# Optimization experiments

Hardware: AMD Instinct MI355X
Metric: run time of the kernel (lower is better)

Reference implementation:

```python
import jax, jax.numpy as jnp
import numpy as np

N_T, N_C, N_M = 300000, 100000, 20000
D_IN, D, D_OUT = 390, 128, 64
H_PRE, H_POST = 256, 64


def _nrm(k, shape, scale=0.02):
    return jax.random.normal(k, shape, dtype=jnp.float32) * scale


def setup_inputs() -> dict:
    key = jax.random.key(0)
    ks = jax.random.split(key, 24)
    inp = {
        'input_features': jax.random.normal(ks[0], (N_T, D_IN), jnp.float32),
        'card_of_target': jax.random.randint(ks[1], (N_T,), 0, N_C, jnp.int32),
        'merchant_of_target': jax.random.randint(ks[2], (N_T,), 0, N_M, jnp.int32),
        # HeteroEmbedding tables for src types feeding 'target'
        'card_emb': _nrm(ks[3], (N_C, D)),
        'merch_emb': _nrm(ks[4], (N_M, D)),
        # target_preprocessing FFBlock (390 -> 256 -> 128, n_layers=2)
        'pre_Wi': _nrm(ks[5], (D_IN, H_PRE)), 'pre_bi': jnp.zeros((H_PRE,), jnp.float32),
        'pre_Wh': _nrm(ks[6], (H_PRE, H_PRE)), 'pre_bh': jnp.zeros((H_PRE,), jnp.float32),
        'pre_Wo': _nrm(ks[7], (H_PRE, D)), 'pre_bo': jnp.zeros((D,), jnp.float32),
        # conv1 / conv2: one GraphConv per etype; order:
        # 0=card->target, 1=merchant->target, 2=target->card, 3=target->merchant
        'conv1_W': _nrm(ks[8], (4, D, D)), 'conv1_b': jnp.zeros((4, D), jnp.float32),
        'conv2_W': _nrm(ks[9], (4, D, D)), 'conv2_b': jnp.zeros((4, D), jnp.float32),
        # conv3: dst=='target' -> D_OUT; dst!='target' -> 1
        'conv3_Wt': _nrm(ks[10], (2, D, D_OUT)), 'conv3_bt': jnp.zeros((2, D_OUT), jnp.float32),
        'conv3_Wo': _nrm(ks[11], (2, D, 1)), 'conv3_bo': jnp.zeros((2, 1), jnp.float32),
        # target_postprocessing FFBlock (64 -> 64 -> 1, n_layers=2)
        'post_Wi': _nrm(ks[12], (D_OUT, H_POST)), 'post_bi': jnp.zeros((H_POST,), jnp.float32),
        'post_Wh': _nrm(ks[13], (H_POST, H_POST)), 'post_bh': jnp.zeros((H_POST,), jnp.float32),
        'post_Wo': _nrm(ks[14], (H_POST, 1)), 'post_bo': jnp.zeros((1,), jnp.float32),
    }
    return inp


def _ff(x, Wi, bi, Wh, bh, Wo, bo, n_layers=2):
    h = jax.nn.relu(x @ Wi + bi)
    for _ in range(1, n_layers):
        h = jax.nn.relu(h @ Wh + bh)
    return h @ Wo + bo


def _deg(ids, n):
    # degree per node over edge endpoint list, clamped to >= 1 (DGL GraphConv)
    return jnp.maximum(jnp.zeros((n,), jnp.float32).at[ids].add(1.0), 1.0)


def _gconv(x_src, src, dst, n_dst, W, b, d_src, d_dst):
    # DGL GraphConv, norm='both': scale src by out_deg^-1/2, matmul,
    # sum messages onto dst, scale by in_deg^-1/2, add bias.
    h = (x_src * jax.lax.rsqrt(d_src)[:, None]) @ W          # [n_src, out]
    agg = jax.ops.segment_sum(h[src], dst, num_segments=n_dst)
    return agg * jax.lax.rsqrt(d_dst)[:, None] + b


def reference(input_features, card_of_target, merchant_of_target,
              card_emb, merch_emb,
              pre_Wi, pre_bi, pre_Wh, pre_bh, pre_Wo, pre_bo,
              conv1_W, conv1_b, conv2_W, conv2_b,
              conv3_Wt, conv3_bt, conv3_Wo, conv3_bo,
              post_Wi, post_bi, post_Wh, post_bh, post_Wo, post_bo):
    n_t, n_c, n_m = input_features.shape[0], card_emb.shape[0], merch_emb.shape[0]
    t_ids = jnp.arange(n_t, dtype=jnp.int32)
    d_c = _deg(card_of_target, n_c)      # card degree (in/out symmetric here)
    d_m = _deg(merchant_of_target, n_m)  # merchant degree
    d_t = _deg(t_ids, n_t)               # target degree (=1 per etype)

    tf = _ff(input_features, pre_Wi, pre_bi, pre_Wh, pre_bh, pre_Wo, pre_bo)

    # conv1 (HeteroGraphConv, aggregate='sum') + relu
    h1_t = (_gconv(card_emb, card_of_target, t_ids, n_t, conv1_W[0], conv1_b[0], d_c, d_t)
            + _gconv(merch_emb, merchant_of_target, t_ids, n_t, conv1_W[1], conv1_b[1], d_m, d_t))
    h1_c = _gconv(tf, t_ids, card_of_target, n_c, conv1_W[2], conv1_b[2], d_t, d_c)
    h1_m = _gconv(tf, t_ids, merchant_of_target, n_m, conv1_W[3], conv1_b[3], d_t, d_m)
    h1_t, h1_c, h1_m = jax.nn.relu(h1_t), jax.nn.relu(h1_c), jax.nn.relu(h1_m)

    # conv2 applied (conv_layers - 2) = 1 time
    h2_t, h2_c, h2_m = h1_t, h1_c, h1_m
    for _ in range(2, 3):
        n_t2 = (_gconv(h2_c, card_of_target, t_ids, n_t, conv2_W[0], conv2_b[0], d_c, d_t)
                + _gconv(h2_m, merchant_of_target, t_ids, n_t, conv2_W[1], conv2_b[1], d_m, d_t))
        n_c2 = _gconv(h2_t, t_ids, card_of_target, n_c, conv2_W[2], conv2_b[2], d_t, d_c)
        n_m2 = _gconv(h2_t, t_ids, merchant_of_target, n_m, conv2_W[3], conv2_b[3], d_t, d_m)
        h2_t, h2_c, h2_m = jax.nn.relu(n_t2), jax.nn.relu(n_c2), jax.nn.relu(n_m2)

    # conv3: D_OUT into target, 1 into non-target dsts; no relu
    h3_t = (_gconv(h2_c, card_of_target, t_ids, n_t, conv3_Wt[0], conv3_bt[0], d_c, d_t)
            + _gconv(h2_m, merchant_of_target, t_ids, n_t, conv3_Wt[1], conv3_bt[1], d_m, d_t))
    h3_c = _gconv(h2_t, t_ids, card_of_target, n_c, conv3_Wo[0], conv3_bo[0], d_t, d_c)
    h3_m = _gconv(h2_t, t_ids, merchant_of_target, n_m, conv3_Wo[1], conv3_bo[1], d_t, d_m)

    h3_t = _ff(h3_t, post_Wi, post_bi, post_Wh, post_bh, post_Wo, post_bo)
    return h3_t, h3_c, h3_m
```

## Files before the change

### kernel.cpp

```cpp
#include <hip/hip_runtime.h>


#define NT 300000
#define NC 100000
#define NM 20000
#define DIN 390
#define DD 128
#define DOUT 64
#define HPRE 256
#define HPOST 64

typedef _Float16 half8 __attribute__((ext_vector_type(8)));
typedef _Float16 half4v __attribute__((ext_vector_type(4)));
typedef float f32x16 __attribute__((ext_vector_type(16)));
typedef float f32x4 __attribute__((ext_vector_type(4)));

#define LO_SCALE 512.0f
#define LO_INV   (1.0f / 512.0f)

__device__ __forceinline__ void split2(float x, _Float16& h, _Float16& l) {
    _Float16 hh = (_Float16)x;
    h = hh;
    l = (_Float16)((x - (float)hh) * LO_SCALE);
}

__device__ __forceinline__ void gload16(const _Float16* g, _Float16* l) {
    __builtin_amdgcn_global_load_lds(
        (const __attribute__((address_space(1))) void*)g,
        (__attribute__((address_space(3))) void*)l, 16, 0, 0);
}

template<int TN>
__global__ __launch_bounds__(512, 4) void gemm_ps(
    const _Float16* __restrict__ Agh, const _Float16* __restrict__ Agl,
    const _Float16* __restrict__ Bgh, const _Float16* __restrict__ Bgl,
    const float* __restrict__ bias, const float* __restrict__ rowscale,
    _Float16* __restrict__ Ch, _Float16* __restrict__ Cl,
    float* __restrict__ C32,
    int M, int Kpad, int N, int relu)
{
    constexpr int BM = 128;
    constexpr int BN = 64 * TN;
    constexpr int BHALF = BN * 32;
    constexpr int BUFB  = 2 * BHALF;
    constexpr int OFF_B = 24576;
    __shared__ __align__(16) _Float16 smem[OFF_B + 2 * BUFB];

    const int tid  = (int)threadIdx.x;
    const int lane = tid & 63;
    const int wave = tid >> 6;
    const int wm0  = (wave & 3) * 32;
    const int wn0  = (wave >> 2) * 32 * TN;

    const int nbn  = N / BN;
    const int bm   = ((int)blockIdx.x / nbn) * BM;
    const int bn   = ((int)blockIdx.x % nbn) * BN;

    const int srow = lane >> 2;
    const int xc8  = (((lane & 3) ^ ((srow >> 1) & 3)) << 3);
    const size_t a_off = (size_t)(bm + wave * 16 + srow) * Kpad + xc8;
    size_t b_off;
    if constexpr (TN == 2) {
        b_off = (size_t)(bn + wave * 16 + srow) * Kpad + xc8;
    } else {
        b_off = (size_t)(bn + (wave & 3) * 16 + srow) * Kpad + xc8;
    }

    auto stageA = [&](int ab, int k0) {
        _Float16* base = &smem[ab * 8192];
        gload16(Agh + a_off + k0, base + wave * 512);
        gload16(Agl + a_off + k0, base + 4096 + wave * 512);
    };
    auto stageB = [&](int bb, int k0) {
        _Float16* base = &smem[OFF_B + bb * BUFB];
        if constexpr (TN == 2) {
            gload16(Bgh + b_off + k0, base + wave * 512);
            gload16(Bgl + b_off + k0, base + BHALF + wave * 512);
        } else {
            gload16((wave < 4 ? Bgh : Bgl) + b_off + k0,
                    base + (wave < 4 ? 0 : BHALF) + (wave & 3) * 512);
        }
    };

    f32x16 zz;
    #pragma unroll
    for (int i = 0; i < 16; ++i) zz[i] = 0.f;
    f32x16 acc_hh[TN], acc_x[TN];
    #pragma unroll
    for (int t2 = 0; t2 < TN; ++t2) { acc_hh[t2] = zz; acc_x[t2] = zz; }

    const int mlr = lane & 31;
    const int hi5 = lane >> 5;
    const int xr  = (mlr >> 1) & 3;

    const int NS = Kpad >> 5;

    stageB(0, 0);
    stageA(0, 0);
    if (NS > 1) stageA(1, 32);

    int ca = 0, cn = 2;

    for (int t = 0; t < NS; ++t) {
        if (t + 1 < NS) stageB((t + 1) & 1, (t + 1) << 5);
        if (t + 2 < NS) stageA(cn, (t + 2) << 5);

        if (t + 2 < NS) {
            asm volatile("s_waitcnt vmcnt(%0)" :: "n"(TN == 2 ? 6 : 5) : "memory");
        } else if (t + 1 < NS) {
            asm volatile("s_waitcnt vmcnt(%0)" :: "n"(TN == 2 ? 4 : 3) : "memory");
        } else {
            asm volatile("s_waitcnt vmcnt(0)" ::: "memory");
        }
        __builtin_amdgcn_s_barrier();
        __builtin_amdgcn_sched_barrier(0);

        const _Float16* sa = &smem[ca * 8192];
        const _Float16* sb = &smem[OFF_B + (t & 1) * BUFB];
        #pragma unroll
        for (int ks = 0; ks < 2; ++ks) {
            const int xo = (((ks * 2 + hi5) ^ xr) << 3);
            const half8 fah = *(const half8*)&sa[(wm0 + mlr) * 32 + xo];
            const half8 fal = *(const half8*)&sa[4096 + (wm0 + mlr) * 32 + xo];
            half8 fbh[TN], fbl[TN];
            #pragma unroll
            for (int t2 = 0; t2 < TN; ++t2) {
                const int nn = wn0 + t2 * 32 + mlr;
                fbh[t2] = *(const half8*)&sb[nn * 32 + xo];
                fbl[t2] = *(const half8*)&sb[BHALF + nn * 32 + xo];
            }
            #pragma unroll
            for (int t2 = 0; t2 < TN; ++t2) {
                acc_hh[t2] = __builtin_amdgcn_mfma_f32_32x32x16_f16(
                    fah, fbh[t2], acc_hh[t2], 0, 0, 0);
                acc_x[t2] = __builtin_amdgcn_mfma_f32_32x32x16_f16(
                    fah, fbl[t2], acc_x[t2], 0, 0, 0);
                acc_x[t2] = __builtin_amdgcn_mfma_f32_32x32x16_f16(
                    fal, fbh[t2], acc_x[t2], 0, 0, 0);
            }
        }
        __builtin_amdgcn_sched_barrier(0);
        __builtin_amdgcn_s_barrier();

        ca = (ca == 2) ? 0 : ca + 1;
        cn = (cn == 2) ? 0 : cn + 1;
    }

    const int r0 = 4 * hi5;
    #pragma unroll
    for (int t2 = 0; t2 < TN; ++t2) {
        const int gcol = bn + wn0 + t2 * 32 + mlr;
        const float bc = (bias != nullptr) ? bias[gcol] : 0.f;
        #pragma unroll
        for (int r = 0; r < 16; ++r) {
            const int grow = bm + wm0 + (r & 3) + r0 + 8 * (r >> 2);
            if (grow < M) {
                float v = acc_hh[t2][r] + acc_x[t2][r] * LO_INV;
                if (rowscale != nullptr) v *= rowscale[grow];
                v += bc;
                if (relu) v = fmaxf(v, 0.f);
                if (C32 != nullptr) {
                    C32[(size_t)grow * N + gcol] = v;
                } else {
                    _Float16 hh, ll;
                    split2(v, hh, ll);
                    Ch[(size_t)grow * N + gcol] = hh;
                    Cl[(size_t)grow * N + gcol] = ll;
                }
            }
        }
    }
}

template<int TM, int TN, int WGM, int WGN>
__global__ __launch_bounds__(256, 3) void gemm_mfma(
    const float* __restrict__ A, const _Float16* __restrict__ Wh,
    const _Float16* __restrict__ Wl, const float* __restrict__ bias,
    const float* __restrict__ rowscale,
    float* __restrict__ C32, _Float16* __restrict__ Ch, _Float16* __restrict__ Cl,
    int M, int K, int N, int Kpad, int relu)
{
    constexpr int BM = 32 * TM * WGM;
    constexpr int BN = 32 * TN * WGN;
    constexpr int RS = 40;
    __shared__ __align__(16) _Float16 Ah[BM * RS];
    __shared__ __align__(16) _Float16 Al[BM * RS];
    __shared__ __align__(16) _Float16 Bh[BN * RS];
    __shared__ __align__(16) _Float16 Bl[BN * RS];

    const int tid  = (int)threadIdx.x;
    const int lane = tid & 63;
    const int wave = tid >> 6;
    const int wm0 = (wave % WGM) * 32 * TM;
    const int wn0 = (wave / WGM) * 32 * TN;

    const int nbn = N / BN;
    const int tile = (int)blockIdx.x;
    const int bm = (tile / nbn) * BM;
    const int bn = (tile % nbn) * BN;

    f32x16 zz;
    #pragma unroll
    for (int i = 0; i < 16; ++i) zz[i] = 0.f;
    f32x16 acc_hh[TM][TN], acc_x[TM][TN];
    #pragma unroll
    for (int tm = 0; tm < TM; ++tm)
        #pragma unroll
        for (int tn = 0; tn < TN; ++tn) { acc_hh[tm][tn] = zz; acc_x[tm][tn] = zz; }

    constexpr int TPR  = 256 / BM;
    constexpr int KPT  = 32 / TPR;
    constexpr int FQ   = KPT / 4;
    const int sar = tid / TPR;
    const int sak = (tid % TPR) * KPT;
    const int agrow = bm + sar;
    const float* Aptr = A + (size_t)agrow * K;

    constexpr int TPRB = 256 / BN;
    constexpr int KPTB = 32 / TPRB;
    constexpr int NB   = KPTB / 8;
    const int sbr = tid / TPRB;
    const int sbk = (tid % TPRB) * KPTB;
    const _Float16* Bhp = Wh + (size_t)(bn + sbr) * Kpad + sbk;
    const _Float16* Blp = Wl + (size_t)(bn + sbr) * Kpad + sbk;

    const int ml  = lane & 31;
    const int klo = (lane >> 5) * 8;

    f32x4 areg0[FQ], areg1[FQ];
    half8 bh0[NB], bl0[NB], bh1[NB], bl1[NB];

    auto loadA = [&](f32x4 (&ar)[FQ], int k0) {
        #pragma unroll
        for (int q = 0; q < FQ; ++q) {
            const int kb = k0 + sak + q * 4;
            f32x4 f = {0.f, 0.f, 0.f, 0.f};
            if (agrow < M) {
                if (kb + 3 < K) {
                    f = *(const f32x4*)(Aptr + kb);
                } else {
                    if (kb + 0 < K) f[0] = Aptr[kb + 0];
                    if (kb + 1 < K) f[1] = Aptr[kb + 1];
                    if (kb + 2 < K) f[2] = Aptr[kb + 2];
                    if (kb + 3 < K) f[3] = Aptr[kb + 3];
                }
            }
            ar[q] = f;
        }
    };
    auto loadB = [&](half8 (&bh)[NB], half8 (&bl)[NB], int k0) {
        #pragma unroll
        for (int j = 0; j < NB; ++j) {
            bh[j] = *(const half8*)(Bhp + k0 + j * 8);
            bl[j] = *(const half8*)(Blp + k0 + j * 8);
        }
    };

    loadA(areg0, 0);
    loadB(bh0, bl0, 0);
    if (32 < K) { loadA(areg1, 32); loadB(bh1, bl1, 32); }

    auto step = [&](f32x4 (&ar)[FQ], half8 (&bh)[NB], half8 (&bl)[NB], int k0) {
        #pragma unroll
        for (int c = 0; c < FQ / 2; ++c) {
            half8 h, l;
            #pragma unroll
            for (int q = 0; q < 2; ++q) {
                #pragma unroll
                for (int j = 0; j < 4; ++j) {
                    _Float16 th, tl;
                    split2(ar[2 * c + q][j], th, tl);
                    h[q * 4 + j] = th;
                    l[q * 4 + j] = tl;
                }
            }
            *(half8*)&Ah[sar * RS + sak + c * 8] = h;
            *(half8*)&Al[sar * RS + sak + c * 8] = l;
        }
        #pragma unroll
        for (int j = 0; j < NB; ++j) {
            *(half8*)&Bh[sbr * RS + sbk + j * 8] = bh[j];
            *(half8*)&Bl[sbr * RS + sbk + j * 8] = bl[j];
        }
        __syncthreads();

        if (k0 + 64 < K) { loadA(ar, k0 + 64); loadB(bh, bl, k0 + 64); }

        #pragma unroll
        for (int ks = 0; ks < 2; ++ks) {
            const int kk = ks * 16 + klo;
            half8 fah[TM], fal[TM], fbh[TN], fbl[TN];
            #pragma unroll
            for (int t = 0; t < TM; ++t) {
                const int m = wm0 + t * 32 + ml;
                fah[t] = *(const half8*)&Ah[m * RS + kk];
                fal[t] = *(const half8*)&Al[m * RS + kk];
            }
            #pragma unroll
            for (int t = 0; t < TN; ++t) {
                const int n = wn0 + t * 32 + ml;
                fbh[t] = *(const half8*)&Bh[n * RS + kk];
                fbl[t] = *(const half8*)&Bl[n * RS + kk];
            }
            #pragma unroll
            for (int tm = 0; tm < TM; ++tm)
                #pragma unroll
                for (int tn = 0; tn < TN; ++tn) {
                    acc_hh[tm][tn] = __builtin_amdgcn_mfma_f32_32x32x16_f16(
                        fah[tm], fbh[tn], acc_hh[tm][tn], 0, 0, 0);
                    acc_x[tm][tn] = __builtin_amdgcn_mfma_f32_32x32x16_f16(
                        fah[tm], fbl[tn], acc_x[tm][tn], 0, 0, 0);
                    acc_x[tm][tn] = __builtin_amdgcn_mfma_f32_32x32x16_f16(
                        fal[tm], fbh[tn], acc_x[tm][tn], 0, 0, 0);
                }
        }
        __syncthreads();
    };

    for (int k0 = 0; k0 < K; k0 += 64) {
        step(areg0, bh0, bl0, k0);
        if (k0 + 32 < K) step(areg1, bh1, bl1, k0 + 32);
    }

    const int r0 = 4 * (lane >> 5);
    #pragma unroll
    for (int tm = 0; tm < TM; ++tm) {
        #pragma unroll
        for (int tn = 0; tn < TN; ++tn) {
            const int gcol = bn + wn0 + tn * 32 + ml;
            const float bc = (bias != nullptr) ? bias[gcol] : 0.f;
            #pragma unroll
            for (int r = 0; r < 16; ++r) {
                const int grow = bm + wm0 + tm * 32 + (r & 3) + r0 + 8 * (r >> 2);
                if (grow < M) {
                    float v = acc_hh[tm][tn][r] + acc_x[tm][tn][r] * LO_INV;
                    if (rowscale != nullptr) v *= rowscale[grow];
                    v += bc;
                    if (relu) v = fmaxf(v, 0.f);
                    if (C32 != nullptr) {
                        C32[(size_t)grow * N + gcol] = v;
                    } else {
                        _Float16 hh, ll;
                        split2(v, hh, ll);
                        Ch[(size_t)grow * N + gcol] = hh;
                        Cl[(size_t)grow * N + gcol] = ll;
                    }
                }
            }
        }
    }
}

__global__ __launch_bounds__(512, 2) void post_ff(
    const float* __restrict__ hc, const float* __restrict__ hm,
    const int* __restrict__ card, const int* __restrict__ merch,
    const float* __restrict__ bt0, const float* __restrict__ bt1,
    const _Float16* __restrict__ wih, const _Float16* __restrict__ wil,
    const float* __restrict__ bi,
    const _Float16* __restrict__ whh, const _Float16* __restrict__ whl,
    const float* __restrict__ bh,
    const float* __restrict__ wo, const float* __restrict__ bo,
    float* __restrict__ out, int n)
{
    constexpr int SR = 72;
    constexpr int OFF_AH = 0;
    constexpr int OFF_AL = 9216;
    constexpr int OFF_HH = 18432;
    constexpr int OFF_HL = 27648;
    constexpr int OFF_W1H = 36864;
    constexpr int OFF_W1L = 41472;
    constexpr int OFF_W2H = 46080;
    constexpr int OFF_W2L = 50688;
    __shared__ __align__(16) _Float16 S[55296];
    float* sh2 = (float*)&S[OFF_AH];

    const int tid  = (int)threadIdx.x;
    const int lane = tid & 63;
    const int wave = tid >> 6;
    const int bm   = (int)blockIdx.x * 128;

    {
        const int wn = (tid & 255) >> 2;
        const int c0 = (tid & 3) * 16;
        const _Float16* gh = (tid < 256) ? wih : whh;
        const _Float16* gl = (tid < 256) ? wil : whl;
        const int oh = (tid < 256) ? OFF_W1H : OFF_W2H;
        const int ol = (tid < 256) ? OFF_W1L : OFF_W2L;
        *(half8*)&S[oh + wn * SR + c0]     = *(const half8*)(gh + wn * 64 + c0);
        *(half8*)&S[oh + wn * SR + c0 + 8] = *(const half8*)(gh + wn * 64 + c0 + 8);
        *(half8*)&S[ol + wn * SR + c0]     = *(const half8*)(gl + wn * 64 + c0);
        *(half8*)&S[ol + wn * SR + c0 + 8] = *(const half8*)(gl + wn * 64 + c0 + 8);
    }
    {
        const int r  = tid >> 2;
        const int c0 = (tid & 3) << 4;
        const int t  = bm + r;
        const bool ok = (t < n);
        const int ci = ok ? card[t] : 0;
        const int mi = ok ? merch[t] : 0;
        #pragma unroll
        for (int q = 0; q < 4; ++q) {
            const int c = c0 + q * 4;
            float4 a = make_float4(0.f, 0.f, 0.f, 0.f);
            if (ok) {
                float4 va = *(const float4*)(hc + (size_t)ci * 64 + c);
                float4 vb = *(const float4*)(hm + (size_t)mi * 64 + c);
                float4 b0 = *(const float4*)(bt0 + c);
                float4 b1 = *(const float4*)(bt1 + c);
                a.x = va.x + vb.x + b0.x + b1.x;
                a.y = va.y + vb.y + b0.y + b1.y;
                a.z = va.z + vb.z + b0.z + b1.z;
                a.w = va.w + vb.w + b0.w + b1.w;
            }
            half4v h, l;
            _Float16 th, tl;
            split2(a.x, th, tl); h[0] = th; l[0] = tl;
            split2(a.y, th, tl); h[1] = th; l[1] = tl;
            split2(a.z, th, tl); h[2] = th; l[2] = tl;
            split2(a.w, th, tl); h[3] = th; l[3] = tl;
            *(half4v*)&S[OFF_AH + r * SR + c] = h;
            *(half4v*)&S[OFF_AL + r * SR + c] = l;
        }
    }
    __syncthreads();

    const int mlr = lane & 31;
    const int hi5 = lane >> 5;
    const int wm = (wave & 3) * 32;
    const int wn = (wave >> 2) * 32;
    const int r0 = 4 * hi5;

    f32x16 zz;
    #pragma unroll
    for (int i = 0; i < 16; ++i) zz[i] = 0.f;

    {
        f32x16 acc = zz, accx = zz;
        #pragma unroll
        for (int ks = 0; ks < 4; ++ks) {
            const int kk = ks * 16 + hi5 * 8;
            const half8 fah = *(const half8*)&S[OFF_AH + (wm + mlr) * SR + kk];
            const half8 fal = *(const half8*)&S[OFF_AL + (wm + mlr) * SR + kk];
            const half8 fbh = *(const half8*)&S[OFF_W1H + (wn + mlr) * SR + kk];
            const half8 fbl = *(const half8*)&S[OFF_W1L + (wn + mlr) * SR + kk];
            acc  = __builtin_amdgcn_mfma_f32_32x32x16_f16(fah, fbh, acc, 0, 0, 0);
            accx = __builtin_amdgcn_mfma_f32_32x32x16_f16(fah, fbl, accx, 0, 0, 0);
            accx = __builtin_amdgcn_mfma_f32_32x32x16_f16(fal, fbh, accx, 0, 0, 0);
        }
        const float bc = bi[wn + mlr];
        __syncthreads();
        #pragma unroll
        for (int r = 0; r < 16; ++r) {
            const int row = wm + (r & 3) + r0 + 8 * (r >> 2);
            float v = acc[r] + accx[r] * LO_INV + bc;
            v = fmaxf(v, 0.f);
            _Float16 hh, ll;
            split2(v, hh, ll);
            S[OFF_HH + row * SR + wn + mlr] = hh;
            S[OFF_HL + row * SR + wn + mlr] = ll;
        }
    }
    __syncthreads();

    {
        f32x16 acc = zz, accx = zz;
        #pragma unroll
        for (int ks = 0; ks < 4; ++ks) {
            const int kk = ks * 16 + hi5 * 8;
            const half8 fah = *(const half8*)&S[OFF_HH + (wm + mlr) * SR + kk];
            const half8 fal = *(const half8*)&S[OFF_HL + (wm + mlr) * SR + kk];
            const half8 fbh = *(const half8*)&S[OFF_W2H + (wn + mlr) * SR + kk];
            const half8 fbl = *(const half8*)&S[OFF_W2L + (wn + mlr) * SR + kk];
            acc  = __builtin_amdgcn_mfma_f32_32x32x16_f16(fah, fbh, acc, 0, 0, 0);
            accx = __builtin_amdgcn_mfma_f32_32x32x16_f16(fah, fbl, accx, 0, 0, 0);
            accx = __builtin_amdgcn_mfma_f32_32x32x16_f16(fal, fbh, accx, 0, 0, 0);
        }
        const float bc = bh[wn + mlr];
        __syncthreads();
        #pragma unroll
        for (int r = 0; r < 16; ++r) {
            const int row = wm + (r & 3) + r0 + 8 * (r >> 2);
            float v = acc[r] + accx[r] * LO_INV + bc;
            sh2[row * 68 + wn + mlr] = fmaxf(v, 0.f);
        }
    }
    __syncthreads();

    if (tid < 128) {
        const int t = bm + tid;
        if (t < n) {
            float s = bo[0];
            #pragma unroll 8
            for (int c = 0; c < 64; ++c) s += sh2[tid * 68 + c] * wo[c];
            out[t] = s;
        }
    }
}

__global__ void split_w(const float* __restrict__ W, _Float16* __restrict__ hiT,
                        _Float16* __restrict__ loT, int K, int N, int Kpad, int nmat)
{
    int idx = blockIdx.x * blockDim.x + threadIdx.x;
    int total = nmat * N * Kpad;
    if (idx >= total) return;
    int e = idx / (N * Kpad);
    int rem = idx - e * (N * Kpad);
    int n = rem / Kpad;
    int k = rem - n * Kpad;
    float v = (k < K) ? W[((size_t)e * K + k) * N + n] : 0.f;
    _Float16 h = (_Float16)v;
    hiT[idx] = h;
    loT[idx] = (_Float16)((v - (float)h) * LO_SCALE);
}

__global__ void split_a(const float* __restrict__ X, _Float16* __restrict__ xh,
                        _Float16* __restrict__ xl, int M, int Mpad, int K)
{
    int idx = blockIdx.x * blockDim.x + threadIdx.x;
    int per = K >> 3;
    int total = Mpad * per;
    if (idx >= total) return;
    int row = idx / per;
    int k = (idx - row * per) << 3;
    half8 h, l;
    if (row < M) {
        #pragma unroll
        for (int j = 0; j < 8; ++j) {
            _Float16 th, tl;
            split2(X[(size_t)row * K + k + j], th, tl);
            h[j] = th; l[j] = tl;
        }
    } else {
        #pragma unroll
        for (int j = 0; j < 8; ++j) { h[j] = (_Float16)0.f; l[j] = (_Float16)0.f; }
    }
    *(half8*)&xh[(size_t)row * K + k] = h;
    *(half8*)&xl[(size_t)row * K + k] = l;
}

__global__ void count_kernel(const int* __restrict__ card, const int* __restrict__ merch,
                             int* cnt_c, int* cnt_m, int n)
{
    int t = blockIdx.x * blockDim.x + threadIdx.x;
    if (t >= n) return;
    atomicAdd(&cnt_c[card[t]], 1);
    atomicAdd(&cnt_m[merch[t]], 1);
}

__global__ void rsqrt_kernel(const int* __restrict__ cnt, float* __restrict__ rs, int n)
{
    int i = blockIdx.x * blockDim.x + threadIdx.x;
    if (i >= n) return;
    int c = cnt[i];
    if (c < 1) c = 1;
    rs[i] = 1.0f / sqrtf((float)c);
}

__global__ __launch_bounds__(1024) void scan_excl(const int* __restrict__ cnt,
                                                  int* __restrict__ off, int n)
{
    __shared__ int wsum[16];
    const int tid = (int)threadIdx.x;
    const int lane = tid & 63, wid = tid >> 6;
    int carry = 0;
    for (int base = 0; base < n; base += 1024) {
        int i = base + tid;
        int v = (i < n) ? cnt[i] : 0;
        int x = v;
        #pragma unroll
        for (int d = 1; d < 64; d <<= 1) {
            int y = __shfl_up(x, d);
            if (lane >= d) x += y;
        }
        if (lane == 63) wsum[wid] = x;
        __syncthreads();
        int wpre = 0, tot = 0;
        #pragma unroll
        for (int w = 0; w < 16; ++w) {
            int s = wsum[w];
            if (w < wid) wpre += s;
            tot += s;
        }
        if (i < n) off[i] = carry + wpre + (x - v);
        carry += tot;
        __syncthreads();
    }
    if (tid == 0) off[n] = carry;
}

__global__ void fill_sorted(const int* __restrict__ ids, const int* __restrict__ off,
                            int* cur, int* __restrict__ srt, int n)
{
    int t = blockIdx.x * blockDim.x + threadIdx.x;
    if (t >= n) return;
    int c = ids[t];
    int p = atomicAdd(&cur[c], 1);
    srt[off[c] + p] = t;
}

__global__ void gather2_kernel(const float* __restrict__ hc, const float* __restrict__ hm,
                               const int* __restrict__ card, const int* __restrict__ merch,
                               const float* __restrict__ b0, const float* __restrict__ b1,
                               float* __restrict__ out32, _Float16* __restrict__ oh,
                               _Float16* __restrict__ ol, int n, int dim, int relu)
{
    int idx = blockIdx.x * blockDim.x + threadIdx.x;
    int per = dim >> 2;
    int t = idx / per;
    if (t >= n) return;
    int d4 = (idx % per) << 2;
    int c = card[t], m = merch[t];
    float4 a = *(const float4*)(hc + (size_t)c * dim + d4);
    float4 b = *(const float4*)(hm + (size_t)m * dim + d4);
    float4 v0 = *(const float4*)(b0 + d4);
    float4 v1 = *(const float4*)(b1 + d4);
    float4 r;
    r.x = a.x + b.x + v0.x + v1.x;
    r.y = a.y + b.y + v0.y + v1.y;
    r.z = a.z + b.z + v0.z + v1.z;
    r.w = a.w + b.w + v0.w + v1.w;
    if (relu) {
        r.x = fmaxf(r.x, 0.f); r.y = fmaxf(r.y, 0.f);
        r.z = fmaxf(r.z, 0.f); r.w = fmaxf(r.w, 0.f);
    }
    if (out32 != nullptr) {
        *(float4*)(out32 + (size_t)t * dim + d4) = r;
    } else {
        half4v h, l;
        _Float16 th, tl;
        split2(r.x, th, tl); h[0] = th; l[0] = tl;
        split2(r.y, th, tl); h[1] = th; l[1] = tl;
        split2(r.z, th, tl); h[2] = th; l[2] = tl;
        split2(r.w, th, tl); h[3] = th; l[3] = tl;
        *(half4v*)&oh[(size_t)t * dim + d4] = h;
        *(half4v*)&ol[(size_t)t * dim + d4] = l;
    }
}

__global__ __launch_bounds__(256) void agg_csr_kernel(
    const float* __restrict__ proj, int ldp, int doff,
    const int* __restrict__ off, const int* __restrict__ srt,
    const float* __restrict__ rs, const float* __restrict__ bias,
    _Float16* __restrict__ oh, _Float16* __restrict__ ol, int n, int relu)
{
    int node = blockIdx.x * 2 + ((int)threadIdx.x >> 7);
    int d = (int)threadIdx.x & 127;
    if (node >= n) return;
    int s = off[node], e = off[node + 1];
    float acc = 0.f;
    for (int i = s; i < e; ++i) {
        int t = srt[i];
        acc += proj[(size_t)t * ldp + doff + d];
    }
    float v = acc * rs[node] + bias[d];
    if (relu) v = fmaxf(v, 0.f);
    _Float16 hh, ll;
    split2(v, hh, ll);
    oh[(size_t)node * 128 + d] = hh;
    ol[(size_t)node * 128 + d] = ll;
}

__global__ __launch_bounds__(256) void dot2_kernel(
    const float* __restrict__ h, const float* __restrict__ w0,
    const float* __restrict__ w1, float* __restrict__ s2, int n)
{
    int row = blockIdx.x * 4 + ((int)threadIdx.x >> 6);
    int l = (int)threadIdx.x & 63;
    if (row >= n) return;
    const float* x = h + (size_t)row * 128;
    float x0 = x[l], x1 = x[l + 64];
    float p0 = x0 * w0[l] + x1 * w0[l + 64];
    float p1 = x0 * w1[l] + x1 * w1[l + 64];
    #pragma unroll
    for (int o = 32; o > 0; o >>= 1) {
        p0 += __shfl_down(p0, o);
        p1 += __shfl_down(p1, o);
    }
    if (l == 0) { s2[(size_t)row * 2] = p0; s2[(size_t)row * 2 + 1] = p1; }
}

__global__ void agg_scalar_kernel(const float* __restrict__ s2, int which,
                                  const int* __restrict__ off, const int* __restrict__ srt,
                                  const float* __restrict__ rs, const float* __restrict__ bias,
                                  float* __restrict__ out, int n)
{
    int node = blockIdx.x * blockDim.x + threadIdx.x;
    if (node >= n) return;
    float acc = 0.f;
    int e = off[node + 1];
    for (int i = off[node]; i < e; ++i) acc += s2[(size_t)srt[i] * 2 + which];
    out[node] = acc * rs[node] + bias[0];
}

static inline void gemm_ps_launch(const _Float16* Ah, const _Float16* Al,
    const _Float16* Bh, const _Float16* Bl, const float* bias, const float* rs,
    _Float16* Ch, _Float16* Cl, float* C32,
    int M, int Kpad, int N, int relu, hipStream_t s)
{
    const int nbm = (M + 127) / 128;
    if (N % 128 == 0) {
        gemm_ps<2><<<dim3(nbm * (N / 128)), 512, 0, s>>>(
            Ah, Al, Bh, Bl, bias, rs, Ch, Cl, C32, M, Kpad, N, relu);
    } else {
        gemm_ps<1><<<dim3(nbm), 512, 0, s>>>(
            Ah, Al, Bh, Bl, bias, rs, Ch, Cl, C32, M, Kpad, N, relu);
    }
}

#define PAD128(x) ((((x) + 127) / 128) * 128)

extern "C" void kernel_launch(void* const* d_in, const int* in_sizes, int n_in,
                              void* d_out, int out_size, void* d_ws, size_t ws_size,
                              hipStream_t stream)
{
    const float* x_in      = (const float*)d_in[0];
    const int*   card      = (const int*)d_in[1];
    const int*   merch     = (const int*)d_in[2];
    const float* card_emb  = (const float*)d_in[3];
    const float* merch_emb = (const float*)d_in[4];
    const float* pre_Wi = (const float*)d_in[5];
    const float* pre_bi = (const float*)d_in[6];
    const float* pre_Wh = (const float*)d_in[7];
    const float* pre_bh = (const float*)d_in[8];
    const float* pre_Wo = (const float*)d_in[9];
    const float* pre_bo = (const float*)d_in[10];
    const float* conv1_W = (const float*)d_in[11];
    const float* conv1_b = (const float*)d_in[12];
    const float* conv2_W = (const float*)d_in[13];
    const float* conv2_b = (const float*)d_in[14];
    const float* conv3_Wt = (const float*)d_in[15];
    const float* conv3_bt = (const float*)d_in[16];
    const float* conv3_Wo = (const float*)d_in[17];
    const float* conv3_bo = (const float*)d_in[18];
    const float* post_Wi = (const float*)d_in[19];
    const float* post_bi = (const float*)d_in[20];
    const float* post_Wh = (const float*)d_in[21];
    const float* post_bh = (const float*)d_in[22];
    const float* post_Wo = (const float*)d_in[23];
    const float* post_bo = (const float*)d_in[24];

    float* out = (float*)d_out;

    const int MTP = PAD128(NT);
    const int MCP = PAD128(NC);
    const int MMP = PAD128(NM);

    char* ws = (char*)d_ws;
    size_t off = 0;
    auto alloc = [&](size_t bytes) -> char* {
        char* p = ws + off;
        off += (bytes + 255) & ~(size_t)255;
        return p;
    };
    int* cnt_c = (int*)alloc((size_t)NC * 4);
    int* cnt_m = (int*)alloc((size_t)NM * 4);
    int* cur_c = (int*)alloc((size_t)NC * 4);
    int* cur_m = (int*)alloc((size_t)NM * 4);
    size_t zero_bytes = (size_t)((char*)(cur_m + NM) - (char*)cnt_c);
    int* off_c = (int*)alloc((size_t)(NC + 1) * 4);
    int* off_m = (int*)alloc((size_t)(NM + 1) * 4);
    int* srt_c = (int*)alloc((size_t)NT * 4);
    int* srt_m = (int*)alloc((size_t)NT * 4);
    float* rs_c = (float*)alloc((size_t)NC * 4);
    float* rs_m = (float*)alloc((size_t)NM * 4);

    const int KP_WI = 416;
    _Float16* wi_h  = (_Float16*)alloc((size_t)HPRE * KP_WI * 2);
    _Float16* wi_l  = (_Float16*)alloc((size_t)HPRE * KP_WI * 2);
    _Float16* wh_h  = (_Float16*)alloc((size_t)HPRE * HPRE * 2);
    _Float16* wh_l  = (_Float16*)alloc((size_t)HPRE * HPRE * 2);
    _Float16* wo_h  = (_Float16*)alloc((size_t)DD * HPRE * 2);
    _Float16* wo_l  = (_Float16*)alloc((size_t)DD * HPRE * 2);
    _Float16* c1_h  = (_Float16*)alloc((size_t)4 * DD * DD * 2);
    _Float16* c1_l  = (_Float16*)alloc((size_t)4 * DD * DD * 2);
    _Float16* c2_h  = (_Float16*)alloc((size_t)4 * DD * DD * 2);
    _Float16* c2_l  = (_Float16*)alloc((size_t)4 * DD * DD * 2);
    _Float16* c3_h  = (_Float16*)alloc((size_t)2 * DOUT * DD * 2);
    _Float16* c3_l  = (_Float16*)alloc((size_t)2 * DOUT * DD * 2);
    _Float16* pi_h  = (_Float16*)alloc((size_t)HPOST * DOUT * 2);
    _Float16* pi_l  = (_Float16*)alloc((size_t)HPOST * DOUT * 2);
    _Float16* ph_h  = (_Float16*)alloc((size_t)HPOST * HPOST * 2);
    _Float16* ph_l  = (_Float16*)alloc((size_t)HPOST * HPOST * 2);

    _Float16* ce_h   = (_Float16*)alloc((size_t)MCP * DD * 2);
    _Float16* ce_l   = (_Float16*)alloc((size_t)MCP * DD * 2);
    _Float16* me_h   = (_Float16*)alloc((size_t)MMP * DD * 2);
    _Float16* me_l   = (_Float16*)alloc((size_t)MMP * DD * 2);
    _Float16* bufA_h = (_Float16*)alloc((size_t)MTP * HPRE * 2);
    _Float16* bufA_l = (_Float16*)alloc((size_t)MTP * HPRE * 2);
    _Float16* bufB_h = (_Float16*)alloc((size_t)MTP * HPRE * 2);
    _Float16* bufB_l = (_Float16*)alloc((size_t)MTP * HPRE * 2);
    _Float16* tf_h   = (_Float16*)alloc((size_t)MTP * DD * 2);
    _Float16* tf_l   = (_Float16*)alloc((size_t)MTP * DD * 2);
    _Float16* h1t_h  = (_Float16*)alloc((size_t)MTP * DD * 2);
    _Float16* h1t_l  = (_Float16*)alloc((size_t)MTP * DD * 2);
    _Float16* h1c_h  = (_Float16*)alloc((size_t)MCP * DD * 2);
    _Float16* h1c_l  = (_Float16*)alloc((size_t)MCP * DD * 2);
    _Float16* h1m_h  = (_Float16*)alloc((size_t)MMP * DD * 2);
    _Float16* h1m_l  = (_Float16*)alloc((size_t)MMP * DD * 2);
    _Float16* h2c_h  = (_Float16*)alloc((size_t)MCP * DD * 2);
    _Float16* h2c_l  = (_Float16*)alloc((size_t)MCP * DD * 2);
    _Float16* h2m_h  = (_Float16*)alloc((size_t)MMP * DD * 2);
    _Float16* h2m_l  = (_Float16*)alloc((size_t)MMP * DD * 2);

    float* proj = (float*)alloc((size_t)MTP * 256 * 4);
    float* h2_t = (float*)alloc((size_t)MTP * DD * 4);
    float* hc_p = (float*)alloc((size_t)MCP * DD * 4);
    float* hm_p = (float*)alloc((size_t)MMP * DD * 4);
    float* s2   = (float*)alloc((size_t)NT * 2 * 4);
    (void)ws_size; (void)in_sizes; (void)n_in; (void)out_size;

    hipMemsetAsync(cnt_c, 0, zero_bytes, stream);
    count_kernel<<<(NT + 255) / 256, 256, 0, stream>>>(card, merch, cnt_c, cnt_m, NT);
    rsqrt_kernel<<<(NC + 255) / 256, 256, 0, stream>>>(cnt_c, rs_c, NC);
    rsqrt_kernel<<<(NM + 255) / 256, 256, 0, stream>>>(cnt_m, rs_m, NM);
    scan_excl<<<1, 1024, 0, stream>>>(cnt_c, off_c, NC);
    scan_excl<<<1, 1024, 0, stream>>>(cnt_m, off_m, NM);
    fill_sorted<<<(NT + 255) / 256, 256, 0, stream>>>(card, off_c, cur_c, srt_c, NT);
    fill_sorted<<<(NT + 255) / 256, 256, 0, stream>>>(merch, off_m, cur_m, srt_m, NT);

    auto splitw = [&](const float* W, _Float16* h, _Float16* l, int K, int N, int Kpad, int nmat) {
        int total = nmat * N * Kpad;
        split_w<<<(total + 255) / 256, 256, 0, stream>>>(W, h, l, K, N, Kpad, nmat);
    };
    splitw(pre_Wi,   wi_h, wi_l, DIN,  HPRE,  KP_WI, 1);
    splitw(pre_Wh,   wh_h, wh_l, HPRE, HPRE,  HPRE,  1);
    splitw(pre_Wo,   wo_h, wo_l, HPRE, DD,    HPRE,  1);
    splitw(conv1_W,  c1_h, c1_l, DD,   DD,    DD,    4);
    splitw(conv2_W,  c2_h, c2_l, DD,   DD,    DD,    4);
    splitw(conv3_Wt, c3_h, c3_l, DD,   DOUT,  DD,    2);
    splitw(post_Wi,  pi_h, pi_l, DOUT, HPOST, DOUT,  1);
    splitw(post_Wh,  ph_h, ph_l, HPOST,HPOST, HPOST, 1);

    split_a<<<((MCP * (DD / 8)) + 255) / 256, 256, 0, stream>>>(card_emb, ce_h, ce_l, NC, MCP, DD);
    split_a<<<((MMP * (DD / 8)) + 255) / 256, 256, 0, stream>>>(merch_emb, me_h, me_l, NM, MMP, DD);

    const int WP  = DD * DD;
    const int WP3 = DOUT * DD;

    {
        const int nbm = (NT + 63) / 64;
        gemm_mfma<1, 2, 2, 2><<<dim3(nbm * 2), 256, 0, stream>>>(
            x_in, wi_h, wi_l, pre_bi, nullptr, nullptr, bufA_h, bufA_l,
            NT, DIN, HPRE, KP_WI, 1);
    }
    gemm_ps_launch(bufA_h, bufA_l, wh_h, wh_l, pre_bh, nullptr,
                   bufB_h, bufB_l, nullptr, NT, HPRE, HPRE, 1, stream);
    gemm_ps_launch(bufB_h, bufB_l, wo_h, wo_l, pre_bo, nullptr,
                   tf_h, tf_l, nullptr, NT, HPRE, DD, 0, stream);

    gemm_ps_launch(ce_h, ce_l, c1_h + 0 * WP, c1_l + 0 * WP, nullptr, rs_c,
                   nullptr, nullptr, hc_p, NC, DD, DD, 0, stream);
    gemm_ps_launch(me_h, me_l, c1_h + 1 * WP, c1_l + 1 * WP, nullptr, rs_m,
                   nullptr, nullptr, hm_p, NM, DD, DD, 0, stream);
    gather2_kernel<<<(NT * (DD / 4) + 255) / 256, 256, 0, stream>>>(
        hc_p, hm_p, card, merch, conv1_b, conv1_b + DD,
        nullptr, h1t_h, h1t_l, NT, DD, 1);
    gemm_ps_launch(tf_h, tf_l, c1_h + 2 * WP, c1_l + 2 * WP, nullptr, nullptr,
                   nullptr, nullptr, proj, NT, DD, 256, 0, stream);
    agg_csr_kernel<<<(NC + 1) / 2, 256, 0, stream>>>(proj, 256, 0, off_c, srt_c, rs_c,
                                                     conv1_b + 2 * DD, h1c_h, h1c_l, NC, 1);
    agg_csr_kernel<<<(NM + 1) / 2, 256, 0, stream>>>(proj, 256, 128, off_m, srt_m, rs_m,
                                                     conv1_b + 3 * DD, h1m_h, h1m_l, NM, 1);

    gemm_ps_launch(h1c_h, h1c_l, c2_h + 0 * WP, c2_l + 0 * WP, nullptr, rs_c,
                   nullptr, nullptr, hc_p, NC, DD, DD, 0, stream);
    gemm_ps_launch(h1m_h, h1m_l, c2_h + 1 * WP, c2_l + 1 * WP, nullptr, rs_m,
                   nullptr, nullptr, hm_p, NM, DD, DD, 0, stream);
    gather2_kernel<<<(NT * (DD / 4) + 255) / 256, 256, 0, stream>>>(
        hc_p, hm_p, card, merch, conv2_b, conv2_b + DD,
        h2_t, nullptr, nullptr, NT, DD, 1);
    gemm_ps_launch(h1t_h, h1t_l, c2_h + 2 * WP, c2_l + 2 * WP, nullptr, nullptr,
                   nullptr, nullptr, proj, NT, DD, 256, 0, stream);
    agg_csr_kernel<<<(NC + 1) / 2, 256, 0, stream>>>(proj, 256, 0, off_c, srt_c, rs_c,
                                                     conv2_b + 2 * DD, h2c_h, h2c_l, NC, 1);
    agg_csr_kernel<<<(NM + 1) / 2, 256, 0, stream>>>(proj, 256, 128, off_m, srt_m, rs_m,
                                                     conv2_b + 3 * DD, h2m_h, h2m_l, NM, 1);

    gemm_ps_launch(h2c_h, h2c_l, c3_h + 0 * WP3, c3_l + 0 * WP3, nullptr, rs_c,
                   nullptr, nullptr, hc_p, NC, DD, DOUT, 0, stream);
    gemm_ps_launch(h2m_h, h2m_l, c3_h + 1 * WP3, c3_l + 1 * WP3, nullptr, rs_m,
                   nullptr, nullptr, hm_p, NM, DD, DOUT, 0, stream);
    dot2_kernel<<<(NT + 3) / 4, 256, 0, stream>>>(h2_t, conv3_Wo, conv3_Wo + DD, s2, NT);
    agg_scalar_kernel<<<(NC + 255) / 256, 256, 0, stream>>>(s2, 0, off_c, srt_c, rs_c,
                                                            conv3_bo + 0, out + NT, NC);
    agg_scalar_kernel<<<(NM + 255) / 256, 256, 0, stream>>>(s2, 1, off_m, srt_m, rs_m,
                                                            conv3_bo + 1, out + NT + NC, NM);

    post_ff<<<dim3((NT + 127) / 128), 512, 0, stream>>>(
        hc_p, hm_p, card, merch, conv3_bt, conv3_bt + DOUT,
        pi_h, pi_l, post_bi, ph_h, ph_l, post_bh, post_Wo, post_bo, out, NT);
}
```

Baseline: 2.796 ms.

## Aggregate target features before projecting for card/merchant convs, simplify GEMM pipelines

For the target->card and target->merchant graph convolutions, the raw target features are now summed over each destination node's edges first and then multiplied by the weight, instead of projecting all 300k target rows and aggregating the projections. This swaps a 300k-row GEMM with N=256 for two GEMMs over 100k and 20k rows, with bias, row scale and relu applied in the GEMM epilogue. The gathers now read 128-wide fp32 rows and the target features are stored as fp32 rather than split fp16 pairs. Separately, both GEMM kernels drop from triple/double-buffered register and LDS pipelining to a plain double buffer, which may expose more load latency.

```diff
diff --git a/kernel.cpp b/kernel.cpp
--- a/kernel.cpp
+++ b/kernel.cpp
@@ -41,10 +41,12 @@
 {
     constexpr int BM = 128;
     constexpr int BN = 64 * TN;
-    constexpr int BHALF = BN * 32;
-    constexpr int BUFB  = 2 * BHALF;
-    constexpr int OFF_B = 24576;
-    __shared__ __align__(16) _Float16 smem[OFF_B + 2 * BUFB];
+    constexpr int OFF_AL = 4096;
+    constexpr int OFF_BH = 8192;
+    constexpr int OFF_BL = 8192 + BN * 32;
+    constexpr int BUFH   = 8192 + 2 * BN * 32;
+    constexpr int NLD    = (TN == 2) ? 4 : 3;
+    __shared__ __align__(16) _Float16 smem[2 * BUFH];
 
     const int tid  = (int)threadIdx.x;
     const int lane = tid & 63;
@@ -66,19 +68,16 @@
         b_off = (size_t)(bn + (wave & 3) * 16 + srow) * Kpad + xc8;
     }
 
-    auto stageA = [&](int ab, int k0) {
-        _Float16* base = &smem[ab * 8192];
-        gload16(Agh + a_off + k0, base + wave * 512);
-        gload16(Agl + a_off + k0, base + 4096 + wave * 512);
-    };
-    auto stageB = [&](int bb, int k0) {
-        _Float16* base = &smem[OFF_B + bb * BUFB];
+    auto stage = [&](int b, int k0) {
+        _Float16* sb = &smem[b * BUFH];
+        gload16(Agh + a_off + k0, sb + wave * 512);
+        gload16(Agl + a_off + k0, sb + OFF_AL + wave * 512);
         if constexpr (TN == 2) {
-            gload16(Bgh + b_off + k0, base + wave * 512);
-            gload16(Bgl + b_off + k0, base + BHALF + wave * 512);
+            gload16(Bgh + b_off + k0, sb + OFF_BH + wave * 512);
+            gload16(Bgl + b_off + k0, sb + OFF_BL + wave * 512);
         } else {
             gload16((wave < 4 ? Bgh : Bgl) + b_off + k0,
-                    base + (wave < 4 ? 0 : BHALF) + (wave & 3) * 512);
+                    sb + (wave < 4 ? OFF_BH : OFF_BL) + (wave & 3) * 512);
         }
     };
 
@@ -94,40 +93,30 @@
     const int xr  = (mlr >> 1) & 3;
 
     const int NS = Kpad >> 5;
-
-    stageB(0, 0);
-    stageA(0, 0);
-    if (NS > 1) stageA(1, 32);
-
-    int ca = 0, cn = 2;
+    stage(0, 0);
 
     for (int t = 0; t < NS; ++t) {
-        if (t + 1 < NS) stageB((t + 1) & 1, (t + 1) << 5);
-        if (t + 2 < NS) stageA(cn, (t + 2) << 5);
-
-        if (t + 2 < NS) {
-            asm volatile("s_waitcnt vmcnt(%0)" :: "n"(TN == 2 ? 6 : 5) : "memory");
-        } else if (t + 1 < NS) {
-            asm volatile("s_waitcnt vmcnt(%0)" :: "n"(TN == 2 ? 4 : 3) : "memory");
+        if (t + 1 < NS) {
+            stage((t + 1) & 1, (t + 1) << 5);
+            asm volatile("s_waitcnt vmcnt(%0)" :: "n"(NLD) : "memory");
         } else {
             asm volatile("s_waitcnt vmcnt(0)" ::: "memory");
         }
         __builtin_amdgcn_s_barrier();
         __builtin_amdgcn_sched_barrier(0);
 
-        const _Float16* sa = &smem[ca * 8192];
-        const _Float16* sb = &smem[OFF_B + (t & 1) * BUFB];
+        const _Float16* sb = &smem[(t & 1) * BUFH];
         #pragma unroll
         for (int ks = 0; ks < 2; ++ks) {
             const int xo = (((ks * 2 + hi5) ^ xr) << 3);
-            const half8 fah = *(const half8*)&sa[(wm0 + mlr) * 32 + xo];
-            const half8 fal = *(const half8*)&sa[4096 + (wm0 + mlr) * 32 + xo];
+            const half8 fah = *(const half8*)&sb[(wm0 + mlr) * 32 + xo];
+            const half8 fal = *(const half8*)&sb[OFF_AL + (wm0 + mlr) * 32 + xo];
             half8 fbh[TN], fbl[TN];
             #pragma unroll
             for (int t2 = 0; t2 < TN; ++t2) {
                 const int nn = wn0 + t2 * 32 + mlr;
-                fbh[t2] = *(const half8*)&sb[nn * 32 + xo];
-                fbl[t2] = *(const half8*)&sb[BHALF + nn * 32 + xo];
+                fbh[t2] = *(const half8*)&sb[OFF_BH + nn * 32 + xo];
+                fbl[t2] = *(const half8*)&sb[OFF_BL + nn * 32 + xo];
             }
             #pragma unroll
             for (int t2 = 0; t2 < TN; ++t2) {
@@ -141,9 +130,6 @@
         }
         __builtin_amdgcn_sched_barrier(0);
         __builtin_amdgcn_s_barrier();
-
-        ca = (ca == 2) ? 0 : ca + 1;
-        cn = (cn == 2) ? 0 : cn + 1;
     }
 
     const int r0 = 4 * hi5;
@@ -227,10 +213,10 @@
     const int ml  = lane & 31;
     const int klo = (lane >> 5) * 8;
 
-    f32x4 areg0[FQ], areg1[FQ];
-    half8 bh0[NB], bl0[NB], bh1[NB], bl1[NB];
-
-    auto loadA = [&](f32x4 (&ar)[FQ], int k0) {
+    f32x4 areg[FQ];
+    half8 bhreg[NB], blreg[NB];
+
+    auto loadA = [&](int k0) {
         #pragma unroll
         for (int q = 0; q < FQ; ++q) {
             const int kb = k0 + sak + q * 4;
@@ -245,22 +231,21 @@
                     if (kb + 3 < K) f[3] = Aptr[kb + 3];
                 }
             }
-            ar[q] = f;
+            areg[q] = f;
         }
     };
-    auto loadB = [&](half8 (&bh)[NB], half8 (&bl)[NB], int k0) {
+    auto loadB = [&](int k0) {
         #pragma unroll
         for (int j = 0; j < NB; ++j) {
-            bh[j] = *(const half8*)(Bhp + k0 + j * 8);
-            bl[j] = *(const half8*)(Blp + k0 + j * 8);
+            bhreg[j] = *(const half8*)(Bhp + k0 + j * 8);
+            blreg[j] = *(const half8*)(Blp + k0 + j * 8);
         }
     };
 
-    loadA(areg0, 0);
-    loadB(bh0, bl0, 0);
-    if (32 < K) { loadA(areg1, 32); loadB(bh1, bl1, 32); }
-
-    auto step = [&](f32x4 (&ar)[FQ], half8 (&bh)[NB], half8 (&bl)[NB], int k0) {
+    loadA(0);
+    loadB(0);
+
+    for (int k0 = 0; k0 < K; k0 += 32) {
         #pragma unroll
         for (int c = 0; c < FQ / 2; ++c) {
             half8 h, l;
@@ -269,7 +254,7 @@
                 #pragma unroll
                 for (int j = 0; j < 4; ++j) {
                     _Float16 th, tl;
-                    split2(ar[2 * c + q][j], th, tl);
+                    split2(areg[2 * c + q][j], th, tl);
                     h[q * 4 + j] = th;
                     l[q * 4 + j] = tl;
                 }
@@ -279,12 +264,12 @@
         }
         #pragma unroll
         for (int j = 0; j < NB; ++j) {
-            *(half8*)&Bh[sbr * RS + sbk + j * 8] = bh[j];
-            *(half8*)&Bl[sbr * RS + sbk + j * 8] = bl[j];
+            *(half8*)&Bh[sbr * RS + sbk + j * 8] = bhreg[j];
+            *(half8*)&Bl[sbr * RS + sbk + j * 8] = blreg[j];
         }
         __syncthreads();
 
-        if (k0 + 64 < K) { loadA(ar, k0 + 64); loadB(bh, bl, k0 + 64); }
+        if (k0 + 32 < K) { loadA(k0 + 32); loadB(k0 + 32); }
 
         #pragma unroll
         for (int ks = 0; ks < 2; ++ks) {
@@ -315,11 +300,6 @@
                 }
         }
         __syncthreads();
-    };
-
-    for (int k0 = 0; k0 < K; k0 += 64) {
-        step(areg0, bh0, bl0, k0);
-        if (k0 + 32 < K) step(areg1, bh1, bl1, k0 + 32);
     }
 
     const int r0 = 4 * (lane >> 5);
@@ -601,8 +581,7 @@
 __global__ void gather2_kernel(const float* __restrict__ hc, const float* __restrict__ hm,
                                const int* __restrict__ card, const int* __restrict__ merch,
                                const float* __restrict__ b0, const float* __restrict__ b1,
-                               float* __restrict__ out32, _Float16* __restrict__ oh,
-                               _Float16* __restrict__ ol, int n, int dim, int relu)
+                               float* __restrict__ out, int n, int dim, int relu)
 {
     int idx = blockIdx.x * blockDim.x + threadIdx.x;
     int per = dim >> 2;
@@ -623,39 +602,23 @@
         r.x = fmaxf(r.x, 0.f); r.y = fmaxf(r.y, 0.f);
         r.z = fmaxf(r.z, 0.f); r.w = fmaxf(r.w, 0.f);
     }
-    if (out32 != nullptr) {
-        *(float4*)(out32 + (size_t)t * dim + d4) = r;
-    } else {
-        half4v h, l;
-        _Float16 th, tl;
-        split2(r.x, th, tl); h[0] = th; l[0] = tl;
-        split2(r.y, th, tl); h[1] = th; l[1] = tl;
-        split2(r.z, th, tl); h[2] = th; l[2] = tl;
-        split2(r.w, th, tl); h[3] = th; l[3] = tl;
-        *(half4v*)&oh[(size_t)t * dim + d4] = h;
-        *(half4v*)&ol[(size_t)t * dim + d4] = l;
-    }
-}
-
-__global__ __launch_bounds__(256) void agg_csr_kernel(
-    const float* __restrict__ proj, int ldp, int doff,
-    const int* __restrict__ off, const int* __restrict__ srt,
-    const float* __restrict__ rs, const float* __restrict__ bias,
-    _Float16* __restrict__ oh, _Float16* __restrict__ ol, int n, int relu)
+    *(float4*)(out + (size_t)t * dim + d4) = r;
+}
+
+__global__ __launch_bounds__(256) void agg_raw_kernel(
+    const float* __restrict__ src, const int* __restrict__ off,
+    const int* __restrict__ srt, _Float16* __restrict__ oh,
+    _Float16* __restrict__ ol, int n)
 {
     int node = blockIdx.x * 2 + ((int)threadIdx.x >> 7);
     int d = (int)threadIdx.x & 127;
     if (node >= n) return;
     int s = off[node], e = off[node + 1];
     float acc = 0.f;
-    for (int i = s; i < e; ++i) {
-        int t = srt[i];
-        acc += proj[(size_t)t * ldp + doff + d];
-    }
-    float v = acc * rs[node] + bias[d];
-    if (relu) v = fmaxf(v, 0.f);
+    for (int i = s; i < e; ++i)
+        acc += src[(size_t)srt[i] * 128 + d];
     _Float16 hh, ll;
-    split2(v, hh, ll);
+    split2(acc, hh, ll);
     oh[(size_t)node * 128 + d] = hh;
     ol[(size_t)node * 128 + d] = ll;
 }
@@ -790,10 +753,10 @@
     _Float16* bufA_l = (_Float16*)alloc((size_t)MTP * HPRE * 2);
     _Float16* bufB_h = (_Float16*)alloc((size_t)MTP * HPRE * 2);
     _Float16* bufB_l = (_Float16*)alloc((size_t)MTP * HPRE * 2);
-    _Float16* tf_h   = (_Float16*)alloc((size_t)MTP * DD * 2);
-    _Float16* tf_l   = (_Float16*)alloc((size_t)MTP * DD * 2);
-    _Float16* h1t_h  = (_Float16*)alloc((size_t)MTP * DD * 2);
-    _Float16* h1t_l  = (_Float16*)alloc((size_t)MTP * DD * 2);
+    _Float16* agC_h  = (_Float16*)alloc((size_t)MCP * DD * 2);
+    _Float16* agC_l  = (_Float16*)alloc((size_t)MCP * DD * 2);
+    _Float16* agM_h  = (_Float16*)alloc((size_t)MMP * DD * 2);
+    _Float16* agM_l  = (_Float16*)alloc((size_t)MMP * DD * 2);
     _Float16* h1c_h  = (_Float16*)alloc((size_t)MCP * DD * 2);
     _Float16* h1c_l  = (_Float16*)alloc((size_t)MCP * DD * 2);
     _Float16* h1m_h  = (_Float16*)alloc((size_t)MMP * DD * 2);
@@ -803,7 +766,8 @@
     _Float16* h2m_h  = (_Float16*)alloc((size_t)MMP * DD * 2);
     _Float16* h2m_l  = (_Float16*)alloc((size_t)MMP * DD * 2);
 
-    float* proj = (float*)alloc((size_t)MTP * 256 * 4);
+    float* tf   = (float*)alloc((size_t)MTP * DD * 4);
+    float* h1_t = (float*)alloc((size_t)MTP * DD * 4);
     float* h2_t = (float*)alloc((size_t)MTP * DD * 4);
     float* hc_p = (float*)alloc((size_t)MCP * DD * 4);
     float* hm_p = (float*)alloc((size_t)MMP * DD * 4);
@@ -847,35 +811,33 @@
     gemm_ps_launch(bufA_h, bufA_l, wh_h, wh_l, pre_bh, nullptr,
                    bufB_h, bufB_l, nullptr, NT, HPRE, HPRE, 1, stream);
     gemm_ps_launch(bufB_h, bufB_l, wo_h, wo_l, pre_bo, nullptr,
-                   tf_h, tf_l, nullptr, NT, HPRE, DD, 0, stream);
+                   nullptr, nullptr, tf, NT, HPRE, DD, 0, stream);
 
     gemm_ps_launch(ce_h, ce_l, c1_h + 0 * WP, c1_l + 0 * WP, nullptr, rs_c,
                    nullptr, nullptr, hc_p, NC, DD, DD, 0, stream);
     gemm_ps_launch(me_h, me_l, c1_h + 1 * WP, c1_l + 1 * WP, nullptr, rs_m,
                    nullptr, nullptr, hm_p, NM, DD, DD, 0, stream);
     gather2_kernel<<<(NT * (DD / 4) + 255) / 256, 256, 0, stream>>>(
-        hc_p, hm_p, card, merch, conv1_b, conv1_b + DD,
-        nullptr, h1t_h, h1t_l, NT, DD, 1);
-    gemm_ps_launch(tf_h, tf_l, c1_h + 2 * WP, c1_l + 2 * WP, nullptr, nullptr,
-                   nullptr, nullptr, proj, NT, DD, 256, 0, stream);
-    agg_csr_kernel<<<(NC + 1) / 2, 256, 0, stream>>>(proj, 256, 0, off_c, srt_c, rs_c,
-                                                     conv1_b + 2 * DD, h1c_h, h1c_l, NC, 1);
-    agg_csr_kernel<<<(NM + 1) / 2, 256, 0, stream>>>(proj, 256, 128, off_m, srt_m, rs_m,
-                                                     conv1_b + 3 * DD, h1m_h, h1m_l, NM, 1);
+        hc_p, hm_p, card, merch, conv1_b, conv1_b + DD, h1_t, NT, DD, 1);
+    agg_raw_kernel<<<(NC + 1) / 2, 256, 0, stream>>>(tf, off_c, srt_c, agC_h, agC_l, NC);
+    agg_raw_kernel<<<(NM + 1) / 2, 256, 0, stream>>>(tf, off_m, srt_m, agM_h, agM_l, NM);
+    gemm_ps_launch(agC_h, agC_l, c1_h + 2 * WP, c1_l + 2 * WP, conv1_b + 2 * DD, rs_c,
+                   h1c_h, h1c_l, nullptr, NC, DD, DD, 1, stream);
+    gemm_ps_launch(agM_h, agM_l, c1_h + 3 * WP, c1_l + 3 * WP, conv1_b + 3 * DD, rs_m,
+                   h1m_h, h1m_l, nullptr, NM, DD, DD, 1, stream);
 
     gemm_ps_launch(h1c_h, h1c_l, c2_h + 0 * WP, c2_l + 0 * WP, nullptr, rs_c,
                    nullptr, nullptr, hc_p, NC, DD, DD, 0, stream);
     gemm_ps_launch(h1m_h, h1m_l, c2_h + 1 * WP, c2_l + 1 * WP, nullptr, rs_m,
                    nullptr, nullptr, hm_p, NM, DD, DD, 0, stream);
     gather2_kernel<<<(NT * (DD / 4) + 255) / 256, 256, 0, stream>>>(
-        hc_p, hm_p, card, merch, conv2_b, conv2_b + DD,
-        h2_t, nullptr, nullptr, NT, DD, 1);
-    gemm_ps_launch(h1t_h, h1t_l, c2_h + 2 * WP, c2_l + 2 * WP, nullptr, nullptr,
-                   nullptr, nullptr, proj, NT, DD, 256, 0, stream);
-    agg_csr_kernel<<<(NC + 1) / 2, 256, 0, stream>>>(proj, 256, 0, off_c, srt_c, rs_c,
-                                                     conv2_b + 2 * DD, h2c_h, h2c_l, NC, 1);
-    agg_csr_kernel<<<(NM + 1) / 2, 256, 0, stream>>>(proj, 256, 128, off_m, srt_m, rs_m,
-                                                     conv2_b + 3 * DD, h2m_h, h2m_l, NM, 1);
+        hc_p, hm_p, card, merch, conv2_b, conv2_b + DD, h2_t, NT, DD, 1);
+    agg_raw_kernel<<<(NC + 1) / 2, 256, 0, stream>>>(h1_t, off_c, srt_c, agC_h, agC_l, NC);
+    agg_raw_kernel<<<(NM + 1) / 2, 256, 0, stream>>>(h1_t, off_m, srt_m, agM_h, agM_l, NM);
+    gemm_ps_launch(agC_h, agC_l, c2_h + 2 * WP, c2_l + 2 * WP, conv2_b + 2 * DD, rs_c,
+                   h2c_h, h2c_l, nullptr, NC, DD, DD, 1, stream);
+    gemm_ps_launch(agM_h, agM_l, c2_h + 3 * WP, c2_l + 3 * WP, conv2_b + 3 * DD, rs_m,
+                   h2m_h, h2m_l, nullptr, NM, DD, DD, 1, stream);
 
     gemm_ps_launch(h2c_h, h2c_l, c3_h + 0 * WP3, c3_l + 0 * WP3, nullptr, rs_c,
                    nullptr, nullptr, hc_p, NC, DD, DOUT, 0, stream);
```

Result: faster. 2.492 ms (-10.9%).
